# Kernel tuning notes

Hardware: AMD Instinct MI355X
Metric: run time of the kernel (lower is better)

## Reference

```python
import jax, jax.numpy as jnp
import numpy as np

B, L, DIM, H, D = 4, 1024, 1024, 8, 32


def setup_inputs() -> dict:
    key = jax.random.key(0)
    ks = jax.random.split(key, 8)
    s = 0.02
    return dict(
        x=jax.random.normal(ks[0], (B, L, DIM), jnp.float32),
        W_in=jax.random.normal(ks[1], (DIM, DIM), jnp.float32) * s,
        b_in=jnp.zeros((DIM,), jnp.float32),
        W_qkva=jax.random.normal(ks[2], (H * D * 8, DIM), jnp.float32) * s,
        b_qkva=jnp.zeros((H * D * 8,), jnp.float32),
        W_y=jax.random.normal(ks[3], (DIM, H * D * 2), jnp.float32) * s,
        b_y=jnp.zeros((DIM,), jnp.float32),
        W_out=jax.random.normal(ks[4], (DIM, DIM), jnp.float32) * s,
        b_out=jnp.zeros((DIM,), jnp.float32),
        h0_re=jax.random.normal(ks[5], (H, D, D), jnp.float32),
        h0_im=jax.random.normal(ks[6], (H, D, D), jnp.float32),
    )


def reference(x, W_in, b_in, W_qkva, b_qkva, W_y, b_y, W_out, b_out, h0_re, h0_im):
    b, Ls, dim = x.shape
    Hh, Dd = h0_re.shape[0], h0_re.shape[1]
    u = jax.nn.silu(x @ W_in.T + b_in)
    qkva = (u @ W_qkva.T + b_qkva).reshape(b, Ls, Hh, Dd, 4, 2)
    c = jax.lax.complex(qkva[..., 0], qkva[..., 1])  # [b,L,H,D,4] complex
    q, k, v, a = c[..., 0], c[..., 1], c[..., 2], c[..., 3]
    mag2 = a.real * a.real + a.imag * a.imag
    # unit-modulus rotation scaled by sigmoid(log|a|^2) gate
    a = a * (jax.lax.rsqrt(mag2) * jax.nn.sigmoid(jnp.log(mag2)))
    kv = jnp.einsum('blhd,blhe->blhde', k, v)  # [b,L,H,D,D] complex
    h0 = jax.lax.complex(h0_re, h0_im)[None]  # [1,H,D,D]
    # fold initial state into step 0: h_0 = a_0 * h_init + kv_0
    kv = kv.at[:, 0].add(a[:, 0, ..., None] * h0)
    a_e = a[..., None]  # [b,L,H,D,1], broadcasts over state col dim

    def comb(c1, c2):
        a1, x1 = c1
        a2, x2 = c2
        return (a1 * a2, a2 * x1 + x2)

    # linear recurrence h_l = a_l * h_{l-1} + kv_l (equiv. to the FFT/cumsum
    # triangular-product matrix in the original module)
    _, h = jax.lax.associative_scan(comb, (a_e, kv), axis=1)
    y = jnp.einsum('blhd,blhde->blhe', q, h)  # [b,L,H,D] complex
    y2 = jnp.stack([y.real, y.imag], axis=-1).reshape(b, Ls, Hh * Dd * 2)
    y2 = jax.nn.silu(y2 @ W_y.T + b_y)
    return y2 @ W_out.T + b_out
```

## Files before the change

kernel.cpp:

```cpp
#include <hip/hip_runtime.h>

#define B_ 4
#define L_ 1024
#define DIM_ 1024
#define H_ 8
#define D_ 32
#define LSEG 32
#define NSEG (L_/LSEG)

typedef __bf16 bf16_t;
typedef __bf16 bf16x8 __attribute__((ext_vector_type(8)));
typedef float f32x4 __attribute__((ext_vector_type(4)));

__device__ __forceinline__ void gload_lds16(const bf16_t* g, bf16_t* l) {
  __builtin_amdgcn_global_load_lds((const __attribute__((address_space(1))) void*)g,
                                   (__attribute__((address_space(3))) void*)l, 16, 0, 0);
}
__device__ __forceinline__ void gload_lds16f(const float* g, float* l) {
  __builtin_amdgcn_global_load_lds((const __attribute__((address_space(1))) void*)g,
                                   (__attribute__((address_space(3))) void*)l, 16, 0, 0);
}

__global__ __launch_bounds__(256) void cvt_all(const float* __restrict__ x,
                                               const float* __restrict__ w1,
                                               const float* __restrict__ w2,
                                               const float* __restrict__ w3,
                                               const float* __restrict__ w4,
                                               bf16_t* __restrict__ ox,
                                               bf16_t* __restrict__ o1,
                                               bf16_t* __restrict__ o2,
                                               bf16_t* __restrict__ o3,
                                               bf16_t* __restrict__ o4) {
  int g = blockIdx.x;
  const float* in; bf16_t* out; int i;
  if      (g < 4096) { in = x;  out = ox; i = g * 256 + threadIdx.x; }
  else if (g < 5120) { in = w1; out = o1; i = (g - 4096) * 256 + threadIdx.x; }
  else if (g < 7168) { in = w2; out = o2; i = (g - 5120) * 256 + threadIdx.x; }
  else if (g < 7680) { in = w3; out = o3; i = (g - 7168) * 256 + threadIdx.x; }
  else               { in = w4; out = o4; i = (g - 7680) * 256 + threadIdx.x; }
  float4 v = ((const float4*)in)[i];
  union { bf16_t b[4]; unsigned long long q; } pk;
  pk.b[0] = (bf16_t)v.x; pk.b[1] = (bf16_t)v.y;
  pk.b[2] = (bf16_t)v.z; pk.b[3] = (bf16_t)v.w;
  ((unsigned long long*)out)[i] = pk.q;
}

template<int BN, int ACT, int OUTBF, int GATE>
__global__ __launch_bounds__(256) void gemm_nt(const bf16_t* __restrict__ A,
                                               const bf16_t* __restrict__ Bm,
                                               const float* __restrict__ bias,
                                               void* __restrict__ Cout,
                                               int M, int N, int K) {
  constexpr int NI = BN / 32;
  constexpr int ISS_B = BN / 32;
  __shared__ __align__(16) bf16_t As[128 * 64];
  __shared__ __align__(16) bf16_t Bs[BN * 64];
  const int t = threadIdx.x;
  const int wid = t >> 6, lane = t & 63;
  const int wr = wid >> 1, wc = wid & 1;
  const int lr = lane & 15, lq = lane >> 4;
  const int bm = blockIdx.x, bn = blockIdx.y;
  const int rA = wid * 32 + (lane >> 3);
  const int rB = wid * (BN / 4) + (lane >> 3);
  const int c8 = (((lane & 7) ^ ((lane >> 3) & 7))) * 8;
  const bf16_t* Ag = A + (size_t)(bm * 128 + rA) * K + c8;
  const bf16_t* Bg = Bm + (size_t)(bn * BN + rB) * K + c8;
  bf16_t* AsW = As + (wid * 32) * 64;
  bf16_t* BsW = Bs + (wid * (BN / 4)) * 64;
  f32x4 acc[4][NI] = {};
  for (int k0 = 0; k0 < K; k0 += 64) {
#pragma unroll
    for (int j = 0; j < 4; ++j)
      gload_lds16(Ag + (size_t)j * 8 * K, AsW + j * 8 * 64);
#pragma unroll
    for (int j = 0; j < ISS_B; ++j)
      gload_lds16(Bg + (size_t)j * 8 * K, BsW + j * 8 * 64);
    Ag += 64; Bg += 64;
    __syncthreads();
#pragma unroll
    for (int ks = 0; ks < 2; ++ks) {
      const int sg = ks * 4 + lq;
      const int sl = (sg ^ (lr & 7)) * 8;
      bf16x8 af[4], bfv[NI];
#pragma unroll
      for (int mi = 0; mi < 4; ++mi)
        af[mi] = *(const bf16x8*)&As[(wr * 64 + mi * 16 + lr) * 64 + sl];
#pragma unroll
      for (int ni = 0; ni < NI; ++ni)
        bfv[ni] = *(const bf16x8*)&Bs[(wc * (BN/2) + ni * 16 + lr) * 64 + sl];
#pragma unroll
      for (int mi = 0; mi < 4; ++mi)
#pragma unroll
        for (int ni = 0; ni < NI; ++ni)
          acc[mi][ni] = __builtin_amdgcn_mfma_f32_16x16x32_bf16(af[mi], bfv[ni], acc[mi][ni], 0, 0, 0);
    }
    __syncthreads();
  }
#pragma unroll
  for (int mi = 0; mi < 4; ++mi) {
#pragma unroll
    for (int ni = 0; ni < NI; ++ni) {
      int colg = bn * BN + wc * (BN/2) + ni * 16 + lr;
      float bb = bias[colg];
#pragma unroll
      for (int r = 0; r < 4; ++r) {
        int rowg = bm * 128 + wr * 64 + mi * 16 + lq * 4 + r;
        float v = acc[mi][ni][r] + bb;
        if (ACT == 1) v = v / (1.0f + __expf(-v));
        if (GATE) {
          float wv = __shfl_xor(v, 1);
          if ((colg & 7) >= 6) {
            float m2 = v * v + wv * wv;
            v *= sqrtf(m2) / (1.0f + m2);
          }
        }
        if (OUTBF) ((bf16_t*)Cout)[(size_t)rowg * N + colg] = (bf16_t)v;
        else       ((float*)Cout)[(size_t)rowg * N + colg] = v;
      }
    }
  }
}

template<int ACT, int OUTBF>
__global__ __launch_bounds__(256) void gemm_nt64(const bf16_t* __restrict__ A,
                                                 const bf16_t* __restrict__ Bm,
                                                 const float* __restrict__ bias,
                                                 void* __restrict__ Cout,
                                                 int M, int N, int K) {
  __shared__ __align__(16) bf16_t As[128 * 128];
  __shared__ __align__(16) bf16_t Bs[64 * 128];
  const int t = threadIdx.x;
  const int wid = t >> 6, lane = t & 63;
  const int wr = wid >> 1, wc = wid & 1;
  const int lr = lane & 15, lq = lane >> 4;
  const int bm = blockIdx.x, bn = blockIdx.y;
  const int crow = wid * 4 + (lane >> 4);
  const int c8 = ((lane & 15) ^ crow) * 8;
  const bf16_t* Ag = A + (size_t)(bm * 128 + crow) * K + c8;
  const bf16_t* Bg = Bm + (size_t)(bn * 64 + crow) * K + c8;
  bf16_t* AsW = As + (wid * 4) * 128;
  bf16_t* BsW = Bs + (wid * 4) * 128;
  f32x4 acc[4][2] = {};
  for (int k0 = 0; k0 < K; k0 += 128) {
#pragma unroll
    for (int j = 0; j < 8; ++j)
      gload_lds16(Ag + (size_t)j * 16 * K, AsW + j * 16 * 128);
#pragma unroll
    for (int j = 0; j < 4; ++j)
      gload_lds16(Bg + (size_t)j * 16 * K, BsW + j * 16 * 128);
    Ag += 128; Bg += 128;
    __syncthreads();
#pragma unroll
    for (int ks = 0; ks < 4; ++ks) {
      const int sg = ks * 4 + lq;
      const int sl = (sg ^ lr) * 8;
      bf16x8 af[4], bfv[2];
#pragma unroll
      for (int mi = 0; mi < 4; ++mi)
        af[mi] = *(const bf16x8*)&As[(wr * 64 + mi * 16 + lr) * 128 + sl];
#pragma unroll
      for (int ni = 0; ni < 2; ++ni)
        bfv[ni] = *(const bf16x8*)&Bs[(wc * 32 + ni * 16 + lr) * 128 + sl];
#pragma unroll
      for (int mi = 0; mi < 4; ++mi)
#pragma unroll
        for (int ni = 0; ni < 2; ++ni)
          acc[mi][ni] = __builtin_amdgcn_mfma_f32_16x16x32_bf16(af[mi], bfv[ni], acc[mi][ni], 0, 0, 0);
    }
    __syncthreads();
  }
#pragma unroll
  for (int mi = 0; mi < 4; ++mi) {
#pragma unroll
    for (int ni = 0; ni < 2; ++ni) {
      int colg = bn * 64 + wc * 32 + ni * 16 + lr;
      float bb = bias[colg];
#pragma unroll
      for (int r = 0; r < 4; ++r) {
        int rowg = bm * 128 + wr * 64 + mi * 16 + lq * 4 + r;
        float v = acc[mi][ni][r] + bb;
        if (ACT == 1) v = v / (1.0f + __expf(-v));
        if (OUTBF) ((bf16_t*)Cout)[(size_t)rowg * N + colg] = (bf16_t)v;
        else       ((float*)Cout)[(size_t)rowg * N + colg] = v;
      }
    }
  }
}

__global__ __launch_bounds__(256) void scan_seg(const float* __restrict__ qkva,
                                                float* __restrict__ y_loc,
                                                float* __restrict__ qP,
                                                float* __restrict__ Aseg,
                                                float* __restrict__ Hfin) {
  __shared__ __align__(16) float Q[LSEG * 256];
  const int t = threadIdx.x;
  const int seg = blockIdx.x;
  const int s = seg & (NSEG - 1);
  const int bh = seg >> 5;
  const int h = bh & (H_ - 1), b = bh >> 3;
  const int wid = t >> 6, lane = t & 63;
  const int dg = lane & 7, eh = lane >> 3;
  const int e = wid * 8 + eh;
  const float* gb = qkva + ((size_t)(b * L_ + s * LSEG) * H_ + h) * 256;
#pragma unroll
  for (int j = 0; j < 8; ++j) {
    const int l = wid * 8 + j;
    gload_lds16f(gb + (size_t)l * (H_ * 256) + lane * 4, Q + l * 256);
  }
  __syncthreads();
  float hr[4] = {}, hi[4] = {};
  float Pr[4] = {1,1,1,1}, Pi[4] = {0,0,0,0};
  size_t row = ((size_t)(b * L_ + s * LSEG) * H_ + h) * D_;
  for (int l = 0; l < LSEG; ++l) {
    const float* R = Q + l * 256;
    float2 vv = *(const float2*)(R + e * 8 + 4);
    float ytr = 0.f, yti = 0.f;
    float2 qpv[4];
#pragma unroll
    for (int j = 0; j < 4; ++j) {
      const int d = dg + 8 * j;
      float4 qk = *(const float4*)(R + d * 8);
      float2 aa = *(const float2*)(R + d * 8 + 6);
      float nPr = aa.x * Pr[j] - aa.y * Pi[j];
      float nPi = aa.x * Pi[j] + aa.y * Pr[j];
      Pr[j] = nPr; Pi[j] = nPi;
      qpv[j].x = qk.x * nPr - qk.y * nPi;
      qpv[j].y = qk.x * nPi + qk.y * nPr;
      float kvr = qk.z * vv.x - qk.w * vv.y;
      float kvi = qk.z * vv.y + qk.w * vv.x;
      float nhr = aa.x * hr[j] - aa.y * hi[j] + kvr;
      float nhi = aa.x * hi[j] + aa.y * hr[j] + kvi;
      hr[j] = nhr; hi[j] = nhi;
      ytr += qk.x * nhr - qk.y * nhi;
      yti += qk.x * nhi + qk.y * nhr;
    }
    ytr += __shfl_down(ytr, 4); yti += __shfl_down(yti, 4);
    ytr += __shfl_down(ytr, 2); yti += __shfl_down(yti, 2);
    ytr += __shfl_down(ytr, 1); yti += __shfl_down(yti, 1);
    if (dg == 0)
      *(float2*)(y_loc + (row + e) * 2) = make_float2(ytr, yti);
    if (t < 8) {
#pragma unroll
      for (int j = 0; j < 4; ++j)
        *(float2*)(qP + (row + dg + 8 * j) * 2) = qpv[j];
    }
    row += H_ * D_;
  }
  const size_t segb = (size_t)seg * D_;
  if (t < 8) {
#pragma unroll
    for (int j = 0; j < 4; ++j)
      *(float2*)(Aseg + (segb + dg + 8 * j) * 2) = make_float2(Pr[j], Pi[j]);
  }
#pragma unroll
  for (int j = 0; j < 4; ++j)
    *(float2*)(Hfin + ((segb + dg + 8 * j) * D_ + e) * 2) = make_float2(hr[j], hi[j]);
}

__global__ __launch_bounds__(128) void seg_combine(const float* __restrict__ h0re,
                                                   const float* __restrict__ h0im,
                                                   const float* __restrict__ Aseg,
                                                   const float* __restrict__ Hfin,
                                                   float* __restrict__ Hc) {
  const int bh = blockIdx.x >> 3;
  const int eg = blockIdx.x & 7;
  const int h = bh & (H_ - 1);
  const int t = threadIdx.x;
  const int d = t >> 2;
  const int e = eg * 4 + (t & 3);
  float cr = h0re[((size_t)h * D_ + d) * D_ + e];
  float ci = h0im[((size_t)h * D_ + d) * D_ + e];
  const size_t idx0  = ((size_t)bh * NSEG * D_ + d) * D_ + e;
  const size_t aidx0 = (size_t)bh * NSEG * D_ + d;
  float2 Ab[8], Fb[8];
#pragma unroll
  for (int p = 0; p < 8; ++p) {
    Ab[p] = *(const float2*)(Aseg + (aidx0 + (size_t)p * D_) * 2);
    Fb[p] = *(const float2*)(Hfin + (idx0 + (size_t)p * D_ * D_) * 2);
  }
  for (int so = 0; so < NSEG; so += 8) {
#pragma unroll
    for (int p = 0; p < 8; ++p) {
      const int s = so + p;
      float2 A0 = Ab[p], F0 = Fb[p];
      if (so + 8 < NSEG) {
        Ab[p] = *(const float2*)(Aseg + (aidx0 + (size_t)(s + 8) * D_) * 2);
        Fb[p] = *(const float2*)(Hfin + (idx0 + (size_t)(s + 8) * D_ * D_) * 2);
      }
      *(float2*)(Hc + (idx0 + (size_t)s * D_ * D_) * 2) = make_float2(cr, ci);
      float nr = A0.x * cr - A0.y * ci + F0.x;
      float ni = A0.x * ci + A0.y * cr + F0.y;
      cr = nr; ci = ni;
    }
  }
}

__global__ __launch_bounds__(256) void y_correct(const float* __restrict__ y_loc,
                                                 const float* __restrict__ qP,
                                                 const float* __restrict__ Hc,
                                                 bf16_t* __restrict__ y2b) {
  __shared__ __align__(16) float Hs[D_ * D_ * 2];
  const int seg = blockIdx.x;
  const int s = seg & (NSEG - 1);
  const int bh = seg >> 5;
  const int h = bh & (H_ - 1), b = bh >> 3;
  const int t = threadIdx.x;
  const float4* src = (const float4*)(Hc + (size_t)seg * (D_ * D_ * 2));
  ((float4*)Hs)[t] = src[t];
  ((float4*)Hs)[t + 256] = src[t + 256];
  __syncthreads();
  const int ep = (t & 15) * 2;
#pragma unroll
  for (int half = 0; half < 2; ++half) {
    const int l = half * 16 + (t >> 4);
    const int lg = s * LSEG + l;
    const size_t rowc = ((size_t)(b * L_ + lg) * H_ + h) * D_;
    const float* qpr = qP + rowc * 2;
    float4 y0 = *(const float4*)(y_loc + (rowc + ep) * 2);
    float ac_r[2] = {y0.x, y0.z}, ac_i[2] = {y0.y, y0.w};
#pragma unroll 4
    for (int d = 0; d < D_; ++d) {
      float2 p = *(const float2*)(qpr + d * 2);
      float4 hv = *(const float4*)&Hs[(d * D_ + ep) * 2];
      ac_r[0] += p.x * hv.x - p.y * hv.y; ac_i[0] += p.x * hv.y + p.y * hv.x;
      ac_r[1] += p.x * hv.z - p.y * hv.w; ac_i[1] += p.x * hv.w + p.y * hv.z;
    }
    union { bf16_t bv[4]; uint2 q; } pk;
    pk.bv[0] = (bf16_t)ac_r[0]; pk.bv[1] = (bf16_t)ac_i[0];
    pk.bv[2] = (bf16_t)ac_r[1]; pk.bv[3] = (bf16_t)ac_i[1];
    *(uint2*)(y2b + (size_t)(b * L_ + lg) * (H_ * D_ * 2) + (h * D_ + ep) * 2) = pk.q;
  }
}

extern "C" void kernel_launch(void* const* d_in, const int* in_sizes, int n_in,
                              void* d_out, int out_size, void* d_ws, size_t ws_size,
                              hipStream_t stream) {
  const float* x      = (const float*)d_in[0];
  const float* W_in   = (const float*)d_in[1];
  const float* b_in   = (const float*)d_in[2];
  const float* W_qkva = (const float*)d_in[3];
  const float* b_qkva = (const float*)d_in[4];
  const float* W_y    = (const float*)d_in[5];
  const float* b_y    = (const float*)d_in[6];
  const float* W_out  = (const float*)d_in[7];
  const float* b_out  = (const float*)d_in[8];
  const float* h0re   = (const float*)d_in[9];
  const float* h0im   = (const float*)d_in[10];

  char* w = (char*)d_ws;
  const size_t MB = 1ull << 20;
  bf16_t* Wb_in   = (bf16_t*)(w + 0*MB);
  bf16_t* Wb_qkva = (bf16_t*)(w + 2*MB);
  bf16_t* Wb_y    = (bf16_t*)(w + 6*MB);
  bf16_t* Wb_out  = (bf16_t*)(w + 7*MB);
  bf16_t* xb      = (bf16_t*)(w + 9*MB);
  float*  qP      = (float*) (w + 9*MB);
  bf16_t* u       = (bf16_t*)(w + 17*MB);
  float*  y_loc   = (float*) (w + 17*MB);
  float*  qkva    = (float*) (w + 25*MB);
  float*  Hc      = (float*) (w + 25*MB);
  bf16_t* y2b     = (bf16_t*)(w + 41*MB);
  bf16_t* z       = (bf16_t*)(w + 45*MB);
  float*  Aseg    = (float*) (w + 57*MB);
  float*  Hfin    = (float*) (w + 58*MB);

  cvt_all<<<8704, 256, 0, stream>>>(x, W_in, W_qkva, W_y, W_out,
                                    xb, Wb_in, Wb_qkva, Wb_y, Wb_out);

  gemm_nt64<1,1><<<dim3(32, 16), 256, 0, stream>>>(xb, Wb_in, b_in, u, 4096, 1024, 1024);
  gemm_nt<64,0,0,1><<<dim3(32, 32), 256, 0, stream>>>(u, Wb_qkva, b_qkva, qkva, 4096, 2048, 1024);
  scan_seg   <<<1024, 256, 0, stream>>>(qkva, y_loc, qP, Aseg, Hfin);
  seg_combine<<<256,  128, 0, stream>>>(h0re, h0im, Aseg, Hfin, Hc);
  y_correct  <<<1024, 256, 0, stream>>>(y_loc, qP, Hc, y2b);
  gemm_nt64<1,1><<<dim3(32, 16), 256, 0, stream>>>(y2b, Wb_y, b_y, z, 4096, 1024, 512);
  gemm_nt64<0,0><<<dim3(32, 16), 256, 0, stream>>>(z, Wb_out, b_out, (float*)d_out, 4096, 1024, 1024);
}
```

Measured before the change: 219.9 us.

## Shrink GEMM tiles to 64x64 and software-pipeline scan LDS reads

The three 1024-wide GEMMs switch from 128x64 to 64x64 output tiles, doubling the grid to 1024 blocks so all CUs on the MI355X have work, at the cost of less operand reuse per block. The segmented scan kernel now double-buffers its per-step LDS reads in registers, prefetching the next timestep while computing the current one. It also restricts the qP/cumulative-product computation to wavefront 0, where the old code had every wave compute it redundantly. These changes target low occupancy and LDS latency on the sequential scan's critical path.

```diff
diff --git a/kernel.cpp b/kernel.cpp
--- a/kernel.cpp
+++ b/kernel.cpp
@@ -122,12 +122,12 @@
 }
 
 template<int ACT, int OUTBF>
-__global__ __launch_bounds__(256) void gemm_nt64(const bf16_t* __restrict__ A,
-                                                 const bf16_t* __restrict__ Bm,
-                                                 const float* __restrict__ bias,
-                                                 void* __restrict__ Cout,
-                                                 int M, int N, int K) {
-  __shared__ __align__(16) bf16_t As[128 * 128];
+__global__ __launch_bounds__(256) void gemm64k(const bf16_t* __restrict__ A,
+                                               const bf16_t* __restrict__ Bm,
+                                               const float* __restrict__ bias,
+                                               void* __restrict__ Cout,
+                                               int M, int N, int K) {
+  __shared__ __align__(16) bf16_t As[64 * 128];
   __shared__ __align__(16) bf16_t Bs[64 * 128];
   const int t = threadIdx.x;
   const int wid = t >> 6, lane = t & 63;
@@ -136,14 +136,14 @@
   const int bm = blockIdx.x, bn = blockIdx.y;
   const int crow = wid * 4 + (lane >> 4);
   const int c8 = ((lane & 15) ^ crow) * 8;
-  const bf16_t* Ag = A + (size_t)(bm * 128 + crow) * K + c8;
+  const bf16_t* Ag = A + (size_t)(bm * 64 + crow) * K + c8;
   const bf16_t* Bg = Bm + (size_t)(bn * 64 + crow) * K + c8;
   bf16_t* AsW = As + (wid * 4) * 128;
   bf16_t* BsW = Bs + (wid * 4) * 128;
-  f32x4 acc[4][2] = {};
+  f32x4 acc[2][2] = {};
   for (int k0 = 0; k0 < K; k0 += 128) {
 #pragma unroll
-    for (int j = 0; j < 8; ++j)
+    for (int j = 0; j < 4; ++j)
       gload_lds16(Ag + (size_t)j * 16 * K, AsW + j * 16 * 128);
 #pragma unroll
     for (int j = 0; j < 4; ++j)
@@ -154,15 +154,15 @@
     for (int ks = 0; ks < 4; ++ks) {
       const int sg = ks * 4 + lq;
       const int sl = (sg ^ lr) * 8;
-      bf16x8 af[4], bfv[2];
-#pragma unroll
-      for (int mi = 0; mi < 4; ++mi)
-        af[mi] = *(const bf16x8*)&As[(wr * 64 + mi * 16 + lr) * 128 + sl];
+      bf16x8 af[2], bfv[2];
+#pragma unroll
+      for (int mi = 0; mi < 2; ++mi)
+        af[mi] = *(const bf16x8*)&As[(wr * 32 + mi * 16 + lr) * 128 + sl];
 #pragma unroll
       for (int ni = 0; ni < 2; ++ni)
         bfv[ni] = *(const bf16x8*)&Bs[(wc * 32 + ni * 16 + lr) * 128 + sl];
 #pragma unroll
-      for (int mi = 0; mi < 4; ++mi)
+      for (int mi = 0; mi < 2; ++mi)
 #pragma unroll
         for (int ni = 0; ni < 2; ++ni)
           acc[mi][ni] = __builtin_amdgcn_mfma_f32_16x16x32_bf16(af[mi], bfv[ni], acc[mi][ni], 0, 0, 0);
@@ -170,14 +170,14 @@
     __syncthreads();
   }
 #pragma unroll
-  for (int mi = 0; mi < 4; ++mi) {
+  for (int mi = 0; mi < 2; ++mi) {
 #pragma unroll
     for (int ni = 0; ni < 2; ++ni) {
       int colg = bn * 64 + wc * 32 + ni * 16 + lr;
       float bb = bias[colg];
 #pragma unroll
       for (int r = 0; r < 4; ++r) {
-        int rowg = bm * 128 + wr * 64 + mi * 16 + lq * 4 + r;
+        int rowg = bm * 64 + wr * 32 + mi * 16 + lq * 4 + r;
         float v = acc[mi][ni][r] + bb;
         if (ACT == 1) v = v / (1.0f + __expf(-v));
         if (OUTBF) ((bf16_t*)Cout)[(size_t)rowg * N + colg] = (bf16_t)v;
@@ -210,42 +210,66 @@
   __syncthreads();
   float hr[4] = {}, hi[4] = {};
   float Pr[4] = {1,1,1,1}, Pi[4] = {0,0,0,0};
-  size_t row = ((size_t)(b * L_ + s * LSEG) * H_ + h) * D_;
-  for (int l = 0; l < LSEG; ++l) {
+  const size_t row0 = ((size_t)(b * L_ + s * LSEG) * H_ + h) * D_;
+
+  float4 qkA[4], qkB[4];
+  float2 aaA[4], aaB[4];
+  float2 vvA, vvB;
+
+  auto LOADR = [&](int l, float4 (&qk)[4], float2 (&aa)[4], float2& vv) {
     const float* R = Q + l * 256;
-    float2 vv = *(const float2*)(R + e * 8 + 4);
+    vv = *(const float2*)(R + e * 8 + 4);
+#pragma unroll
+    for (int j = 0; j < 4; ++j) {
+      qk[j] = *(const float4*)(R + (dg + 8 * j) * 8);
+      aa[j] = *(const float2*)(R + (dg + 8 * j) * 8 + 6);
+    }
+  };
+
+  auto STEP = [&](int l, float4 (&qk)[4], float2 (&aa)[4], float2& vv) {
+    const size_t rowl = row0 + (size_t)l * (H_ * D_);
     float ytr = 0.f, yti = 0.f;
-    float2 qpv[4];
+    if (wid == 0) {
+      float2 qpv[4];
+#pragma unroll
+      for (int j = 0; j < 4; ++j) {
+        float nPr = aa[j].x * Pr[j] - aa[j].y * Pi[j];
+        float nPi = aa[j].x * Pi[j] + aa[j].y * Pr[j];
+        Pr[j] = nPr; Pi[j] = nPi;
+        qpv[j].x = qk[j].x * nPr - qk[j].y * nPi;
+        qpv[j].y = qk[j].x * nPi + qk[j].y * nPr;
+      }
+      if (lane < 8) {
+#pragma unroll
+        for (int j = 0; j < 4; ++j)
+          *(float2*)(qP + (rowl + dg + 8 * j) * 2) = qpv[j];
+      }
+    }
 #pragma unroll
     for (int j = 0; j < 4; ++j) {
-      const int d = dg + 8 * j;
-      float4 qk = *(const float4*)(R + d * 8);
-      float2 aa = *(const float2*)(R + d * 8 + 6);
-      float nPr = aa.x * Pr[j] - aa.y * Pi[j];
-      float nPi = aa.x * Pi[j] + aa.y * Pr[j];
-      Pr[j] = nPr; Pi[j] = nPi;
-      qpv[j].x = qk.x * nPr - qk.y * nPi;
-      qpv[j].y = qk.x * nPi + qk.y * nPr;
-      float kvr = qk.z * vv.x - qk.w * vv.y;
-      float kvi = qk.z * vv.y + qk.w * vv.x;
-      float nhr = aa.x * hr[j] - aa.y * hi[j] + kvr;
-      float nhi = aa.x * hi[j] + aa.y * hr[j] + kvi;
+      float kvr = qk[j].z * vv.x - qk[j].w * vv.y;
+      float kvi = qk[j].z * vv.y + qk[j].w * vv.x;
+      float nhr = aa[j].x * hr[j] - aa[j].y * hi[j] + kvr;
+      float nhi = aa[j].x * hi[j] + aa[j].y * hr[j] + kvi;
       hr[j] = nhr; hi[j] = nhi;
-      ytr += qk.x * nhr - qk.y * nhi;
-      yti += qk.x * nhi + qk.y * nhr;
+      ytr += qk[j].x * nhr - qk[j].y * nhi;
+      yti += qk[j].x * nhi + qk[j].y * nhr;
     }
     ytr += __shfl_down(ytr, 4); yti += __shfl_down(yti, 4);
     ytr += __shfl_down(ytr, 2); yti += __shfl_down(yti, 2);
     ytr += __shfl_down(ytr, 1); yti += __shfl_down(yti, 1);
     if (dg == 0)
-      *(float2*)(y_loc + (row + e) * 2) = make_float2(ytr, yti);
-    if (t < 8) {
-#pragma unroll
-      for (int j = 0; j < 4; ++j)
-        *(float2*)(qP + (row + dg + 8 * j) * 2) = qpv[j];
-    }
-    row += H_ * D_;
-  }
+      *(float2*)(y_loc + (rowl + e) * 2) = make_float2(ytr, yti);
+  };
+
+  LOADR(0, qkA, aaA, vvA);
+  for (int l = 0; l < LSEG; l += 2) {
+    LOADR(l + 1, qkB, aaB, vvB);
+    STEP(l, qkA, aaA, vvA);
+    LOADR(l + 2 < LSEG ? l + 2 : LSEG - 1, qkA, aaA, vvA);
+    STEP(l + 1, qkB, aaB, vvB);
+  }
+
   const size_t segb = (size_t)seg * D_;
   if (t < 8) {
 #pragma unroll
@@ -367,11 +391,11 @@
   cvt_all<<<8704, 256, 0, stream>>>(x, W_in, W_qkva, W_y, W_out,
                                     xb, Wb_in, Wb_qkva, Wb_y, Wb_out);
 
-  gemm_nt64<1,1><<<dim3(32, 16), 256, 0, stream>>>(xb, Wb_in, b_in, u, 4096, 1024, 1024);
+  gemm64k<1,1><<<dim3(64, 16), 256, 0, stream>>>(xb, Wb_in, b_in, u, 4096, 1024, 1024);
   gemm_nt<64,0,0,1><<<dim3(32, 32), 256, 0, stream>>>(u, Wb_qkva, b_qkva, qkva, 4096, 2048, 1024);
   scan_seg   <<<1024, 256, 0, stream>>>(qkva, y_loc, qP, Aseg, Hfin);
   seg_combine<<<256,  128, 0, stream>>>(h0re, h0im, Aseg, Hfin, Hc);
   y_correct  <<<1024, 256, 0, stream>>>(y_loc, qP, Hc, y2b);
-  gemm_nt64<1,1><<<dim3(32, 16), 256, 0, stream>>>(y2b, Wb_y, b_y, z, 4096, 1024, 512);
-  gemm_nt64<0,0><<<dim3(32, 16), 256, 0, stream>>>(z, Wb_out, b_out, (float*)d_out, 4096, 1024, 1024);
-}
+  gemm64k<1,1><<<dim3(64, 16), 256, 0, stream>>>(y2b, Wb_y, b_y, z, 4096, 1024, 512);
+  gemm64k<0,0><<<dim3(64, 16), 256, 0, stream>>>(z, Wb_out, b_out, (float*)d_out, 4096, 1024, 1024);
+}
```

Result: no change. 222.7 us (+1.3%).
